# Kernel tuning notes

Measured on AMD Instinct MI355X. Metric: run time of the kernel, lower is better.

## Reference

```python
import jax, jax.numpy as jnp
import numpy as np

B, N, D, H, E = 4, 2048, 512, 8, 64  # batch, seq, model dim, heads, head dim
EPS = 1e-6
PAD = -2.0
NEG_INF = -1000000000.0
ROPE_MAX = 2048
ROPE_BASE = 10000.0


def compute_rope_rotations(dim, max_seq_len, base):
    inv_freq = 1.0 / base ** (jnp.arange(0, dim, 2, dtype=jnp.float32) / dim)
    pos = jnp.arange(max_seq_len, dtype=jnp.float32)
    freqs = pos[:, None] * inv_freq[None, :]          # (L, dim/2)
    freqs = jnp.repeat(freqs, 2, axis=-1)             # (L, dim)
    return jnp.cos(freqs), jnp.sin(freqs)


def apply_rope(x, cos, sin):
    # Faithful to the source: positions are indexed along AXIS 1 of x.
    # Since q/k have layout (b, h, n, e), axis 1 is the HEAD axis (source quirk).
    seq = x.shape[1]
    c = cos[:seq][None, :, None, :]
    s = sin[:seq][None, :, None, :]
    x1, x2 = x[..., 0::2], x[..., 1::2]
    ch, sh = c[..., 0::2], s[..., 0::2]
    r1 = x1 * ch - x2 * sh
    r2 = x1 * sh + x2 * ch
    return jnp.stack([r1, r2], axis=-1).reshape(x.shape)


def layer_norm(x, gamma, beta):
    mean = jnp.mean(x, axis=-1, keepdims=True)
    var = jnp.mean(jnp.square(x - mean), axis=-1, keepdims=True)
    return gamma * ((x - mean) / jnp.sqrt(var + EPS)) + beta


def setup_inputs() -> dict:
    key = jax.random.key(0)
    ks = jax.random.split(key, 10)
    x = jax.random.normal(ks[0], (B, N, D), dtype=jnp.float32)
    mask = jnp.where(jax.random.uniform(ks[1], (B, N)) < 0.1, PAD, 1.0).astype(jnp.float32)
    glorot_qkv = float(np.sqrt(6.0 / (D + E)))
    q_proj = jax.random.uniform(ks[2], (H, D, E), minval=-glorot_qkv, maxval=glorot_qkv, dtype=jnp.float32)
    k_proj = jax.random.uniform(ks[3], (H, D, E), minval=-glorot_qkv, maxval=glorot_qkv, dtype=jnp.float32)
    v_proj = jax.random.uniform(ks[4], (H, D, E), minval=-glorot_qkv, maxval=glorot_qkv, dtype=jnp.float32)
    g = jax.random.uniform(ks[5], (H, D, E), minval=-0.05, maxval=0.05, dtype=jnp.float32)
    glorot_out = float(np.sqrt(6.0 / (H * E + D)))
    out_w = jax.random.uniform(ks[6], (H * E, D), minval=-glorot_out, maxval=glorot_out, dtype=jnp.float32)
    out_b = jnp.zeros((D,), dtype=jnp.float32)
    gamma_in = jnp.ones((D,), dtype=jnp.float32)
    beta_in = jnp.zeros((D,), dtype=jnp.float32)
    gamma_out = jnp.ones((D,), dtype=jnp.float32)
    beta_out = jnp.zeros((D,), dtype=jnp.float32)
    rope_cos, rope_sin = compute_rope_rotations(E, ROPE_MAX, ROPE_BASE)
    return dict(x=x, mask=mask, q_proj=q_proj, k_proj=k_proj, v_proj=v_proj, g=g,
                gamma_in=gamma_in, beta_in=beta_in, gamma_out=gamma_out, beta_out=beta_out,
                out_w=out_w, out_b=out_b, rope_cos=rope_cos, rope_sin=rope_sin)


def reference(x, mask, q_proj, k_proj, v_proj, g, gamma_in, beta_in,
              gamma_out, beta_out, out_w, out_b, rope_cos, rope_sin):
    scale = 1.0 / jnp.sqrt(jnp.asarray(E, dtype=x.dtype))
    q_input = layer_norm(x, gamma_in, beta_in)          # self-attention: shared LN input
    mask_bin = jnp.where(mask == PAD, 0.0, 1.0).astype(x.dtype)  # (B, N)
    q = jnp.einsum('bnd,hde->bhne', q_input, q_proj)
    k = jnp.einsum('bmd,hde->bhme', q_input, k_proj)
    v = jnp.einsum('bmd,hde->bhme', q_input, v_proj)
    q = apply_rope(q, rope_cos, rope_sin)
    k = apply_rope(k, rope_cos, rope_sin)
    att = jnp.einsum('bhne,bhme->bhnm', q, k) * scale   # (B, H, N, N)
    amask = mask_bin[:, None, :, None] * mask_bin[:, None, None, :]  # (B,1,N,N)
    att = att + (1.0 - amask) * NEG_INF
    att = jax.nn.softmax(att, axis=-1) * amask
    out = jnp.einsum('bhnm,bhme->bhne', att, v)
    gate = jax.nn.sigmoid(jnp.einsum('bnd,hde->bhne', q_input, g))
    out = out * gate
    out = out.transpose(0, 2, 1, 3).reshape(x.shape[0], x.shape[1], H * E)
    out = out @ out_w + out_b
    out = out + x  # residual
    return layer_norm(out, gamma_out, beta_out)


if __name__ == '__main__':
    inp = setup_inputs()
    y = reference(**inp)
    print(y.shape, y.dtype)
```

## Files before the change

### kernel.cpp

```cpp
#include <hip/hip_runtime.h>
#include <math.h>

#define B_ 4
#define N_ 2048
#define D_ 512
#define H_ 8
#define E_ 64

constexpr float EPS = 1e-6f;
constexpr float PADV = -2.0f;
constexpr float SCL = 0.18033688011112043f;

typedef __attribute__((ext_vector_type(8))) __bf16 bf16x8;
typedef __attribute__((ext_vector_type(4))) float f32x4;

__device__ inline unsigned short f2bf(float f) {
  unsigned u = __builtin_bit_cast(unsigned, f);
  u += 0x7fffu + ((u >> 16) & 1u);
  return (unsigned short)(u >> 16);
}
__device__ inline float bf2f(unsigned short v) {
  unsigned u = ((unsigned)v) << 16;
  return __builtin_bit_cast(float, u);
}

__global__ __launch_bounds__(256) void prep_kernel(
    const float* __restrict__ qp, const float* __restrict__ kp,
    const float* __restrict__ vp, const float* __restrict__ gp,
    const float* __restrict__ ow, ushort* __restrict__ wT,
    ushort* __restrict__ owT) {
  __shared__ float Ls[64][65];
  int t = threadIdx.x;
  const float* src;
  ushort* dst;
  int src_ld, r0, c0;
  if (blockIdx.x < 256) {
    int set = blockIdx.x >> 6, tile = blockIdx.x & 63;
    int h = tile >> 3, dt = tile & 7;
    const float* w = set == 0 ? qp : set == 1 ? kp : set == 2 ? vp : gp;
    src = w + (size_t)h * 512 * 64;
    src_ld = 64;
    r0 = dt * 64;
    c0 = 0;
    dst = wT + ((size_t)set * 512 + h * 64) * 512;
  } else {
    int idx = blockIdx.x - 256;
    src = ow;
    src_ld = 512;
    r0 = (idx >> 3) * 64;
    c0 = (idx & 7) * 64;
    dst = owT;
  }
#pragma unroll
  for (int i = 0; i < 4; i++) {
    int id = t + i * 256;
    int r = id >> 4, c4 = (id & 15) * 4;
    float4 v = *(const float4*)(src + (size_t)(r0 + r) * src_ld + c0 + c4);
    Ls[r][c4] = v.x;
    Ls[r][c4 + 1] = v.y;
    Ls[r][c4 + 2] = v.z;
    Ls[r][c4 + 3] = v.w;
  }
  __syncthreads();
#pragma unroll
  for (int i = 0; i < 4; i++) {
    int id = t + i * 256;
    int c = id >> 4, r4 = (id & 15) * 4;
    ushort4 o;
    o.x = f2bf(Ls[r4][c]);
    o.y = f2bf(Ls[r4 + 1][c]);
    o.z = f2bf(Ls[r4 + 2][c]);
    o.w = f2bf(Ls[r4 + 3][c]);
    *(ushort4*)(dst + (size_t)(c0 + c) * 512 + r0 + r4) = o;
  }
}

__global__ __launch_bounds__(256) void ln_bf16_kernel(
    const float* __restrict__ x, const float* __restrict__ gamma,
    const float* __restrict__ beta, ushort* __restrict__ out) {
  int row = blockIdx.x;
  const float* xr = x + (size_t)row * D_;
  int c0 = threadIdx.x, c1 = threadIdx.x + 256;
  float v0 = xr[c0], v1 = xr[c1];
  __shared__ float red[8];
  int lane = threadIdx.x & 63, wid = threadIdx.x >> 6;
  float s = v0 + v1;
  for (int o = 32; o > 0; o >>= 1) s += __shfl_down(s, o, 64);
  if (lane == 0) red[wid] = s;
  __syncthreads();
  float mean = (red[0] + red[1] + red[2] + red[3]) * (1.0f / D_);
  float d0 = v0 - mean, d1 = v1 - mean;
  float sq = d0 * d0 + d1 * d1;
  for (int o = 32; o > 0; o >>= 1) sq += __shfl_down(sq, o, 64);
  if (lane == 0) red[4 + wid] = sq;
  __syncthreads();
  float var = (red[4] + red[5] + red[6] + red[7]) * (1.0f / D_);
  float rstd = rsqrtf(var + EPS);
  ushort* orow = out + (size_t)row * D_;
  orow[c0] = f2bf(gamma[c0] * (d0 * rstd) + beta[c0]);
  orow[c1] = f2bf(gamma[c1] * (d1 * rstd) + beta[c1]);
}

__global__ __launch_bounds__(256) void ln_kernel(
    const float* __restrict__ x, const float* __restrict__ gamma,
    const float* __restrict__ beta, float* __restrict__ out) {
  int row = blockIdx.x;
  const float* xr = x + (size_t)row * D_;
  int c0 = threadIdx.x, c1 = threadIdx.x + 256;
  float v0 = xr[c0], v1 = xr[c1];
  __shared__ float red[8];
  int lane = threadIdx.x & 63, wid = threadIdx.x >> 6;
  float s = v0 + v1;
  for (int o = 32; o > 0; o >>= 1) s += __shfl_down(s, o, 64);
  if (lane == 0) red[wid] = s;
  __syncthreads();
  float mean = (red[0] + red[1] + red[2] + red[3]) * (1.0f / D_);
  float d0 = v0 - mean, d1 = v1 - mean;
  float sq = d0 * d0 + d1 * d1;
  for (int o = 32; o > 0; o >>= 1) sq += __shfl_down(sq, o, 64);
  if (lane == 0) red[4 + wid] = sq;
  __syncthreads();
  float var = (red[4] + red[5] + red[6] + red[7]) * (1.0f / D_);
  float rstd = rsqrtf(var + EPS);
  float* orow = out + (size_t)row * D_;
  orow[c0] = gamma[c0] * (d0 * rstd) + beta[c0];
  orow[c1] = gamma[c1] * (d1 * rstd) + beta[c1];
}

__global__ __launch_bounds__(256) void proj_kernel(
    const ushort* __restrict__ xbf, const ushort* __restrict__ wT,
    const float* __restrict__ rope_cos, const float* __restrict__ rope_sin,
    ushort* __restrict__ qo, ushort* __restrict__ ko,
    ushort* __restrict__ vTo, ushort* __restrict__ go) {
  int tileM = blockIdx.x;
  int h = blockIdx.y & 7;
  int set = blockIdx.y >> 3;

  __shared__ ushort As[128 * 64];
  __shared__ ushort Bs[64 * 64];

  const int t = threadIdx.x;
  const int w = t >> 6;
  const int lane = t & 63;
  const int quad = lane >> 4;
  const int n15 = lane & 15;

  const ushort* wbase = wT + ((size_t)set * 512 + h * 64) * 512;
  const int bn0 = tileM * 128;

  f32x4 acc[2][4];
#pragma unroll
  for (int mb = 0; mb < 2; mb++)
#pragma unroll
    for (int tt = 0; tt < 4; tt++) acc[mb][tt] = (f32x4){0.f, 0.f, 0.f, 0.f};

  for (int k0 = 0; k0 < 512; k0 += 64) {
    __syncthreads();
#pragma unroll
    for (int i = 0; i < 4; i++) {
      int c = t + i * 256;
      int row = c >> 3, c8 = c & 7;
      *(uint4*)&As[(row << 6) + ((c8 ^ (row & 7)) << 3)] =
          *(const uint4*)(xbf + (size_t)(bn0 + row) * 512 + k0 + (c8 << 3));
    }
#pragma unroll
    for (int i = 0; i < 2; i++) {
      int c = t + i * 256;
      int row = c >> 3, c8 = c & 7;
      *(uint4*)&Bs[(row << 6) + ((c8 ^ (row & 7)) << 3)] =
          *(const uint4*)(wbase + (size_t)row * 512 + k0 + (c8 << 3));
    }
    __syncthreads();
#pragma unroll
    for (int kk = 0; kk < 2; kk++) {
      bf16x8 af[2], bfr[4];
#pragma unroll
      for (int mb = 0; mb < 2; mb++) {
        int m = 32 * w + 16 * mb + n15;
        af[mb] = __builtin_bit_cast(
            bf16x8,
            *(const uint4*)&As[(m << 6) + ((((kk << 2) + quad) ^ (m & 7)) << 3)]);
      }
#pragma unroll
      for (int tt = 0; tt < 4; tt++) {
        int n = 16 * tt + n15;
        bfr[tt] = __builtin_bit_cast(
            bf16x8,
            *(const uint4*)&Bs[(n << 6) + ((((kk << 2) + quad) ^ (n & 7)) << 3)]);
      }
#pragma unroll
      for (int mb = 0; mb < 2; mb++)
#pragma unroll
        for (int tt = 0; tt < 4; tt++)
          acc[mb][tt] = __builtin_amdgcn_mfma_f32_16x16x32_bf16(
              af[mb], bfr[tt], acc[mb][tt], 0, 0, 0);
    }
  }

  const int b = bn0 >> 11;
  const int n_base = bn0 & 2047;
  const int bh = b * H_ + h;
  const size_t bhN = (size_t)bh * N_;

  if (set <= 1) {
    ushort* dst = (set == 0) ? qo : ko;
    const float oscale = (set == 0) ? SCL : 1.0f;
    const float sgn = (n15 & 1) ? 1.f : -1.f;
#pragma unroll
    for (int tt = 0; tt < 4; tt++) {
      int e = 16 * tt + n15;
      float cv = rope_cos[(h << 6) + e];
      float sv = rope_sin[(h << 6) + e];
#pragma unroll
      for (int mb = 0; mb < 2; mb++) {
#pragma unroll
        for (int r = 0; r < 4; r++) {
          float xv = acc[mb][tt][r];
          float pv = __shfl_xor(xv, 1, 64);
          float ov = (xv * cv + sgn * pv * sv) * oscale;
          int n = n_base + 32 * w + 16 * mb + 4 * quad + r;
          dst[((bhN + n) << 6) + e] = f2bf(ov);
        }
      }
    }
  } else if (set == 2) {
#pragma unroll
    for (int tt = 0; tt < 4; tt++) {
      int e = 16 * tt + n15;
#pragma unroll
      for (int mb = 0; mb < 2; mb++) {
        int n0 = n_base + 32 * w + 16 * mb + 4 * quad;
        ushort4 pk;
        pk.x = f2bf(acc[mb][tt][0]);
        pk.y = f2bf(acc[mb][tt][1]);
        pk.z = f2bf(acc[mb][tt][2]);
        pk.w = f2bf(acc[mb][tt][3]);
        *(ushort4*)(vTo + ((size_t)(bh * 64 + e)) * N_ + n0) = pk;
      }
    }
  } else {
#pragma unroll
    for (int tt = 0; tt < 4; tt++) {
      int e = 16 * tt + n15;
#pragma unroll
      for (int mb = 0; mb < 2; mb++) {
#pragma unroll
        for (int r = 0; r < 4; r++) {
          int n = n_base + 32 * w + 16 * mb + 4 * quad + r;
          float sv = 1.0f / (1.0f + __expf(-acc[mb][tt][r]));
          go[((bhN + n) << 6) + e] = f2bf(sv);
        }
      }
    }
  }
}

__global__ __launch_bounds__(512, 4) void attn_kernel(
    const ushort* __restrict__ qb, const ushort* __restrict__ kb,
    const ushort* __restrict__ vT, const ushort* __restrict__ gb,
    const float* __restrict__ mask, ushort* __restrict__ out) {
  int qt = blockIdx.x;
  int bh = blockIdx.y;
  int b = bh >> 3, h = bh & 7;

  __shared__ uint Ksu[64 * 32];
  __shared__ uint Vtsu[66 * 32];
  __shared__ uint Pw[8 * 16 * 36];
  __shared__ __align__(16) float kmb[64];

  const int t = threadIdx.x;
  const int w = t >> 6;
  const int lane = t & 63;
  const int quad = lane >> 4;
  const int n15 = lane & 15;
  const int sw = n15 & 7;

  const size_t bhN = (size_t)bh * N_;
  const size_t bN = (size_t)b * N_;
  const int q0 = qt * 128 + 16 * w;

  bf16x8 qf[2];
  {
    const ushort* qrow = qb + ((bhN + q0 + n15) << 6);
#pragma unroll
    for (int hf = 0; hf < 2; hf++)
      qf[hf] =
          __builtin_bit_cast(bf16x8, *(const uint4*)(qrow + 32 * hf + (quad << 3)));
  }

  if (t < 32) Vtsu[64 * 32 + t] = 0x3f803f80u;

  f32x4 O[4], O5;
  O5 = (f32x4){0.f, 0.f, 0.f, 0.f};
#pragma unroll
  for (int tt = 0; tt < 4; tt++) O[tt] = (f32x4){0.f, 0.f, 0.f, 0.f};

  uint* Pq = &Pw[w * 576];

  for (int m0 = 0; m0 < N_; m0 += 64) {
    __syncthreads();
    {
      int row = t >> 3, c8 = t & 7;
      int dst = row * 32 + ((c8 ^ (row & 7)) << 2);
      *(uint4*)&Ksu[dst] =
          *(const uint4*)(kb + ((bhN + m0 + row) << 6) + (c8 << 3));
      *(uint4*)&Vtsu[dst] =
          *(const uint4*)(vT + (size_t)(bh * 64 + row) * N_ + m0 + (c8 << 3));
    }
    if (t < 16) {
      f32x4 mv = *(const f32x4*)(mask + bN + m0 + 4 * t);
      f32x4 bias;
#pragma unroll
      for (int j = 0; j < 4; j++) bias[j] = (mv[j] == PADV) ? -1e9f : 0.f;
      *(f32x4*)&kmb[4 * t] = bias;
    }
    __syncthreads();

    f32x4 st[4];
#pragma unroll
    for (int tt = 0; tt < 4; tt++)
      st[tt] = *(const f32x4*)&kmb[16 * tt + 4 * quad];
#pragma unroll
    for (int hf = 0; hf < 2; hf++) {
#pragma unroll
      for (int tt = 0; tt < 4; tt++) {
        bf16x8 kf = __builtin_bit_cast(
            bf16x8, *(const uint4*)&Ksu[(16 * tt + n15) * 32 +
                                        (((quad + 4 * hf) ^ sw) << 2)]);
        st[tt] =
            __builtin_amdgcn_mfma_f32_16x16x32_bf16(kf, qf[hf], st[tt], 0, 0, 0);
      }
    }

    int rowb = n15 * 36;
#pragma unroll
    for (int tt = 0; tt < 4; tt++) {
      uint u0 = __builtin_bit_cast(
                    uint, __builtin_exp2f(fminf(st[tt][0], 60.f))) + 0x8000u;
      uint u1 = __builtin_bit_cast(
                    uint, __builtin_exp2f(fminf(st[tt][1], 60.f))) + 0x8000u;
      uint u2 = __builtin_bit_cast(
                    uint, __builtin_exp2f(fminf(st[tt][2], 60.f))) + 0x8000u;
      uint u3 = __builtin_bit_cast(
                    uint, __builtin_exp2f(fminf(st[tt][3], 60.f))) + 0x8000u;
      int a = rowb + ((2 * tt + (quad >> 1)) << 2) + ((quad & 1) << 1);
      Pq[a] = __builtin_amdgcn_perm(u1, u0, 0x07060302u);
      Pq[a + 1] = __builtin_amdgcn_perm(u3, u2, 0x07060302u);
    }
    __asm__ volatile("" ::: "memory");

#pragma unroll
    for (int hf = 0; hf < 2; hf++) {
      bf16x8 pf = __builtin_bit_cast(
          bf16x8, *(const uint4*)&Pq[n15 * 36 + ((quad + 4 * hf) << 2)]);
      bf16x8 lf = __builtin_bit_cast(
          bf16x8, *(const uint4*)&Vtsu[64 * 32 + ((quad + 4 * hf) << 2)]);
      O5 = __builtin_amdgcn_mfma_f32_16x16x32_bf16(pf, lf, O5, 0, 0, 0);
#pragma unroll
      for (int tt = 0; tt < 4; tt++) {
        bf16x8 vf = __builtin_bit_cast(
            bf16x8, *(const uint4*)&Vtsu[(16 * tt + n15) * 32 +
                                         (((quad + 4 * hf) ^ sw) << 2)]);
        O[tt] =
            __builtin_amdgcn_mfma_f32_16x16x32_bf16(pf, vf, O[tt], 0, 0, 0);
      }
    }
  }

#pragma unroll
  for (int r = 0; r < 4; r++) {
    int n = q0 + 4 * quad + r;
    float qm = (mask[bN + n] == PADV) ? 0.f : 1.f;
    float inv = qm / fmaxf(O5[r], 1e-30f);
    const ushort* grow = gb + ((bhN + n) << 6);
    ushort* orow = out + ((bN + n) << 9) + (h << 6);
#pragma unroll
    for (int tt = 0; tt < 4; tt++) {
      int e = 16 * tt + n15;
      orow[e] = f2bf(O[tt][r] * inv * bf2f(grow[e]));
    }
  }
}

__global__ __launch_bounds__(256) void outproj_kernel(
    const ushort* __restrict__ ain, const ushort* __restrict__ owT,
    const float* __restrict__ bias, const float* __restrict__ xres,
    float* __restrict__ out) {
  int tileM = blockIdx.x;
  int cc0 = blockIdx.y * 64;

  __shared__ ushort As[128 * 64];
  __shared__ ushort Bs[64 * 64];

  const int t = threadIdx.x;
  const int w = t >> 6;
  const int lane = t & 63;
  const int quad = lane >> 4;
  const int n15 = lane & 15;

  const ushort* wbase = owT + (size_t)cc0 * 512;
  const int bn0 = tileM * 128;

  f32x4 acc[2][4];
#pragma unroll
  for (int mb = 0; mb < 2; mb++)
#pragma unroll
    for (int tt = 0; tt < 4; tt++) acc[mb][tt] = (f32x4){0.f, 0.f, 0.f, 0.f};

  for (int k0 = 0; k0 < 512; k0 += 64) {
    __syncthreads();
#pragma unroll
    for (int i = 0; i < 4; i++) {
      int c = t + i * 256;
      int row = c >> 3, c8 = c & 7;
      *(uint4*)&As[(row << 6) + ((c8 ^ (row & 7)) << 3)] =
          *(const uint4*)(ain + (size_t)(bn0 + row) * 512 + k0 + (c8 << 3));
    }
#pragma unroll
    for (int i = 0; i < 2; i++) {
      int c = t + i * 256;
      int row = c >> 3, c8 = c & 7;
      *(uint4*)&Bs[(row << 6) + ((c8 ^ (row & 7)) << 3)] =
          *(const uint4*)(wbase + (size_t)row * 512 + k0 + (c8 << 3));
    }
    __syncthreads();
#pragma unroll
    for (int kk = 0; kk < 2; kk++) {
      bf16x8 af[2], bfr[4];
#pragma unroll
      for (int mb = 0; mb < 2; mb++) {
        int m = 32 * w + 16 * mb + n15;
        af[mb] = __builtin_bit_cast(
            bf16x8,
            *(const uint4*)&As[(m << 6) + ((((kk << 2) + quad) ^ (m & 7)) << 3)]);
      }
#pragma unroll
      for (int tt = 0; tt < 4; tt++) {
        int n = 16 * tt + n15;
        bfr[tt] = __builtin_bit_cast(
            bf16x8,
            *(const uint4*)&Bs[(n << 6) + ((((kk << 2) + quad) ^ (n & 7)) << 3)]);
      }
#pragma unroll
      for (int mb = 0; mb < 2; mb++)
#pragma unroll
        for (int tt = 0; tt < 4; tt++)
          acc[mb][tt] = __builtin_amdgcn_mfma_f32_16x16x32_bf16(
              af[mb], bfr[tt], acc[mb][tt], 0, 0, 0);
    }
  }

#pragma unroll
  for (int tt = 0; tt < 4; tt++) {
    int c = cc0 + 16 * tt + n15;
    float bv = bias[c];
#pragma unroll
    for (int mb = 0; mb < 2; mb++) {
#pragma unroll
      for (int r = 0; r < 4; r++) {
        size_t row = bn0 + 32 * w + 16 * mb + 4 * quad + r;
        out[row * 512 + c] = acc[mb][tt][r] + bv + xres[row * 512 + c];
      }
    }
  }
}

extern "C" void kernel_launch(void* const* d_in, const int* in_sizes, int n_in,
                              void* d_out, int out_size, void* d_ws,
                              size_t ws_size, hipStream_t stream) {
  (void)in_sizes; (void)n_in; (void)out_size; (void)ws_size;
  const float* x = (const float*)d_in[0];
  const float* mask = (const float*)d_in[1];
  const float* q_proj = (const float*)d_in[2];
  const float* k_proj = (const float*)d_in[3];
  const float* v_proj = (const float*)d_in[4];
  const float* g = (const float*)d_in[5];
  const float* gamma_in = (const float*)d_in[6];
  const float* beta_in = (const float*)d_in[7];
  const float* gamma_out = (const float*)d_in[8];
  const float* beta_out = (const float*)d_in[9];
  const float* out_w = (const float*)d_in[10];
  const float* out_b = (const float*)d_in[11];
  const float* rope_cos = (const float*)d_in[12];
  const float* rope_sin = (const float*)d_in[13];

  char* p = (char*)d_ws;
  ushort* xbf   = (ushort*)p; p += (size_t)8 << 20;
  ushort* wT    = (ushort*)p; p += (size_t)2 << 20;
  ushort* owT   = (ushort*)p; p += (size_t)1 << 20;
  ushort* qb16  = (ushort*)p; p += (size_t)8 << 20;
  ushort* kb16  = (ushort*)p; p += (size_t)8 << 20;
  ushort* vT16  = (ushort*)p; p += (size_t)8 << 20;
  ushort* gate  = (ushort*)p; p += (size_t)8 << 20;
  ushort* attnb = (ushort*)p; p += (size_t)8 << 20;
  float* ypre   = (float*)p;  p += (size_t)16 << 20;

  prep_kernel<<<320, 256, 0, stream>>>(q_proj, k_proj, v_proj, g, out_w, wT,
                                       owT);

  ln_bf16_kernel<<<B_ * N_, 256, 0, stream>>>(x, gamma_in, beta_in, xbf);

  dim3 gp(64, 32);
  proj_kernel<<<gp, 256, 0, stream>>>(xbf, wT, rope_cos, rope_sin, qb16, kb16,
                                      vT16, gate);

  dim3 ga(16, 32);
  attn_kernel<<<ga, 512, 0, stream>>>(qb16, kb16, vT16, gate, mask, attnb);

  dim3 go(64, 8);
  outproj_kernel<<<go, 256, 0, stream>>>(attnb, owT, out_b, x, ypre);

  ln_kernel<<<B_ * N_, 256, 0, stream>>>(ypre, gamma_out, beta_out,
                                         (float*)d_out);
}
```

Baseline: 216.1 us.

## Split attention KV range across two warp groups with 32-row query tiles per warp

Each warp now handles two 16-row query blocks (32 rows), so every K/V fragment read from shared memory feeds two MFMAs instead of one. The 8 warps form two groups that each process half of the key sequence with their own K/V tiles, and the partial outputs and row sums are combined through shared memory at the end. The ones vector for the row-sum MFMA moves into registers instead of a shared-memory row. This halves shared-memory fragment traffic per MFMA and the loop count per block, at the cost of more accumulator registers, an extra reduction step, and an epilogue where half the warps sit idle.

```diff
diff --git a/kernel.cpp b/kernel.cpp
--- a/kernel.cpp
+++ b/kernel.cpp
@@ -13,6 +13,7 @@
 
 typedef __attribute__((ext_vector_type(8))) __bf16 bf16x8;
 typedef __attribute__((ext_vector_type(4))) float f32x4;
+typedef __attribute__((ext_vector_type(8))) unsigned short u16x8;
 
 __device__ inline unsigned short f2bf(float f) {
   unsigned u = __builtin_bit_cast(unsigned, f);
@@ -263,121 +264,184 @@
   int bh = blockIdx.y;
   int b = bh >> 3, h = bh & 7;
 
-  __shared__ uint Ksu[64 * 32];
-  __shared__ uint Vtsu[66 * 32];
-  __shared__ uint Pw[8 * 16 * 36];
-  __shared__ __align__(16) float kmb[64];
+  __shared__ __align__(16) uint arena[12928];
 
   const int t = threadIdx.x;
   const int w = t >> 6;
+  const int grp = w >> 2;
+  const int gw = w & 3;
   const int lane = t & 63;
   const int quad = lane >> 4;
   const int n15 = lane & 15;
   const int sw = n15 & 7;
+  const int tg = t & 255;
+
+  uint* Ks = &arena[grp * 4096];
+  uint* Vts = &arena[grp * 4096 + 2048];
+  uint* Pq = &arena[8192 + w * 576];
+  float* kmbf = (float*)&arena[12800];
 
   const size_t bhN = (size_t)bh * N_;
   const size_t bN = (size_t)b * N_;
-  const int q0 = qt * 128 + 16 * w;
-
-  bf16x8 qf[2];
+  const int q0 = qt * 128 + 32 * gw;
+  const int koff = grp << 10;
+
+  bf16x8 qf[2][2];
+#pragma unroll
+  for (int mb = 0; mb < 2; mb++) {
+    const ushort* qrow = qb + ((bhN + q0 + 16 * mb + n15) << 6);
+#pragma unroll
+    for (int hf = 0; hf < 2; hf++)
+      qf[mb][hf] = __builtin_bit_cast(
+          bf16x8, *(const uint4*)(qrow + 32 * hf + (quad << 3)));
+  }
+
+  bf16x8 ones;
   {
-    const ushort* qrow = qb + ((bhN + q0 + n15) << 6);
-#pragma unroll
-    for (int hf = 0; hf < 2; hf++)
-      qf[hf] =
-          __builtin_bit_cast(bf16x8, *(const uint4*)(qrow + 32 * hf + (quad << 3)));
-  }
-
-  if (t < 32) Vtsu[64 * 32 + t] = 0x3f803f80u;
-
-  f32x4 O[4], O5;
-  O5 = (f32x4){0.f, 0.f, 0.f, 0.f};
-#pragma unroll
-  for (int tt = 0; tt < 4; tt++) O[tt] = (f32x4){0.f, 0.f, 0.f, 0.f};
-
-  uint* Pq = &Pw[w * 576];
-
-  for (int m0 = 0; m0 < N_; m0 += 64) {
+    u16x8 ou;
+#pragma unroll
+    for (int j = 0; j < 8; j++) ou[j] = 0x3F80;
+    ones = __builtin_bit_cast(bf16x8, ou);
+  }
+
+  f32x4 O[2][4], O5[2];
+#pragma unroll
+  for (int mb = 0; mb < 2; mb++) {
+    O5[mb] = (f32x4){0.f, 0.f, 0.f, 0.f};
+#pragma unroll
+    for (int tt = 0; tt < 4; tt++) O[mb][tt] = (f32x4){0.f, 0.f, 0.f, 0.f};
+  }
+
+  for (int it = 0; it < 16; it++) {
+    int m0 = koff + (it << 6);
     __syncthreads();
-    {
-      int row = t >> 3, c8 = t & 7;
+#pragma unroll
+    for (int i = 0; i < 2; i++) {
+      int idx = tg + (i << 8);
+      int row = idx >> 3, c8 = idx & 7;
       int dst = row * 32 + ((c8 ^ (row & 7)) << 2);
-      *(uint4*)&Ksu[dst] =
+      *(uint4*)&Ks[dst] =
           *(const uint4*)(kb + ((bhN + m0 + row) << 6) + (c8 << 3));
-      *(uint4*)&Vtsu[dst] =
+      *(uint4*)&Vts[dst] =
           *(const uint4*)(vT + (size_t)(bh * 64 + row) * N_ + m0 + (c8 << 3));
     }
-    if (t < 16) {
-      f32x4 mv = *(const f32x4*)(mask + bN + m0 + 4 * t);
+    if (tg < 16) {
+      f32x4 mv = *(const f32x4*)(mask + bN + m0 + 4 * tg);
       f32x4 bias;
 #pragma unroll
       for (int j = 0; j < 4; j++) bias[j] = (mv[j] == PADV) ? -1e9f : 0.f;
-      *(f32x4*)&kmb[4 * t] = bias;
+      *(f32x4*)&kmbf[(grp << 6) + 4 * tg] = bias;
     }
     __syncthreads();
 
-    f32x4 st[4];
+    f32x4 bias[4];
 #pragma unroll
     for (int tt = 0; tt < 4; tt++)
-      st[tt] = *(const f32x4*)&kmb[16 * tt + 4 * quad];
+      bias[tt] = *(const f32x4*)&kmbf[(grp << 6) + 16 * tt + 4 * quad];
+
+    f32x4 st[2][4];
+#pragma unroll
+    for (int mb = 0; mb < 2; mb++)
+#pragma unroll
+      for (int tt = 0; tt < 4; tt++) st[mb][tt] = bias[tt];
 #pragma unroll
     for (int hf = 0; hf < 2; hf++) {
 #pragma unroll
       for (int tt = 0; tt < 4; tt++) {
         bf16x8 kf = __builtin_bit_cast(
-            bf16x8, *(const uint4*)&Ksu[(16 * tt + n15) * 32 +
-                                        (((quad + 4 * hf) ^ sw) << 2)]);
-        st[tt] =
-            __builtin_amdgcn_mfma_f32_16x16x32_bf16(kf, qf[hf], st[tt], 0, 0, 0);
-      }
-    }
-
-    int rowb = n15 * 36;
-#pragma unroll
-    for (int tt = 0; tt < 4; tt++) {
-      uint u0 = __builtin_bit_cast(
-                    uint, __builtin_exp2f(fminf(st[tt][0], 60.f))) + 0x8000u;
-      uint u1 = __builtin_bit_cast(
-                    uint, __builtin_exp2f(fminf(st[tt][1], 60.f))) + 0x8000u;
-      uint u2 = __builtin_bit_cast(
-                    uint, __builtin_exp2f(fminf(st[tt][2], 60.f))) + 0x8000u;
-      uint u3 = __builtin_bit_cast(
-                    uint, __builtin_exp2f(fminf(st[tt][3], 60.f))) + 0x8000u;
-      int a = rowb + ((2 * tt + (quad >> 1)) << 2) + ((quad & 1) << 1);
-      Pq[a] = __builtin_amdgcn_perm(u1, u0, 0x07060302u);
-      Pq[a + 1] = __builtin_amdgcn_perm(u3, u2, 0x07060302u);
-    }
-    __asm__ volatile("" ::: "memory");
+            bf16x8, *(const uint4*)&Ks[(16 * tt + n15) * 32 +
+                                       (((quad + 4 * hf) ^ sw) << 2)]);
+        st[0][tt] = __builtin_amdgcn_mfma_f32_16x16x32_bf16(kf, qf[0][hf],
+                                                            st[0][tt], 0, 0, 0);
+        st[1][tt] = __builtin_amdgcn_mfma_f32_16x16x32_bf16(kf, qf[1][hf],
+                                                            st[1][tt], 0, 0, 0);
+      }
+    }
+
+    bf16x8 pf[2][2];
+#pragma unroll
+    for (int mb = 0; mb < 2; mb++) {
+      int rowb = n15 * 36;
+#pragma unroll
+      for (int tt = 0; tt < 4; tt++) {
+        uint u0 = __builtin_bit_cast(
+                      uint, __builtin_exp2f(fminf(st[mb][tt][0], 60.f))) +
+                  0x8000u;
+        uint u1 = __builtin_bit_cast(
+                      uint, __builtin_exp2f(fminf(st[mb][tt][1], 60.f))) +
+                  0x8000u;
+        uint u2 = __builtin_bit_cast(
+                      uint, __builtin_exp2f(fminf(st[mb][tt][2], 60.f))) +
+                  0x8000u;
+        uint u3 = __builtin_bit_cast(
+                      uint, __builtin_exp2f(fminf(st[mb][tt][3], 60.f))) +
+                  0x8000u;
+        int a = rowb + ((2 * tt + (quad >> 1)) << 2) + ((quad & 1) << 1);
+        Pq[a] = __builtin_amdgcn_perm(u1, u0, 0x07060302u);
+        Pq[a + 1] = __builtin_amdgcn_perm(u3, u2, 0x07060302u);
+      }
+      __asm__ volatile("" ::: "memory");
+#pragma unroll
+      for (int hf = 0; hf < 2; hf++)
+        pf[mb][hf] = __builtin_bit_cast(
+            bf16x8, *(const uint4*)&Pq[n15 * 36 + ((quad + 4 * hf) << 2)]);
+      __asm__ volatile("" ::: "memory");
+    }
 
 #pragma unroll
     for (int hf = 0; hf < 2; hf++) {
-      bf16x8 pf = __builtin_bit_cast(
-          bf16x8, *(const uint4*)&Pq[n15 * 36 + ((quad + 4 * hf) << 2)]);
-      bf16x8 lf = __builtin_bit_cast(
-          bf16x8, *(const uint4*)&Vtsu[64 * 32 + ((quad + 4 * hf) << 2)]);
-      O5 = __builtin_amdgcn_mfma_f32_16x16x32_bf16(pf, lf, O5, 0, 0, 0);
+      O5[0] = __builtin_amdgcn_mfma_f32_16x16x32_bf16(pf[0][hf], ones, O5[0],
+                                                      0, 0, 0);
+      O5[1] = __builtin_amdgcn_mfma_f32_16x16x32_bf16(pf[1][hf], ones, O5[1],
+                                                      0, 0, 0);
 #pragma unroll
       for (int tt = 0; tt < 4; tt++) {
         bf16x8 vf = __builtin_bit_cast(
-            bf16x8, *(const uint4*)&Vtsu[(16 * tt + n15) * 32 +
-                                         (((quad + 4 * hf) ^ sw) << 2)]);
-        O[tt] =
-            __builtin_amdgcn_mfma_f32_16x16x32_bf16(pf, vf, O[tt], 0, 0, 0);
-      }
-    }
-  }
-
-#pragma unroll
-  for (int r = 0; r < 4; r++) {
-    int n = q0 + 4 * quad + r;
-    float qm = (mask[bN + n] == PADV) ? 0.f : 1.f;
-    float inv = qm / fmaxf(O5[r], 1e-30f);
-    const ushort* grow = gb + ((bhN + n) << 6);
-    ushort* orow = out + ((bN + n) << 9) + (h << 6);
-#pragma unroll
-    for (int tt = 0; tt < 4; tt++) {
-      int e = 16 * tt + n15;
-      orow[e] = f2bf(O[tt][r] * inv * bf2f(grow[e]));
+            bf16x8, *(const uint4*)&Vts[(16 * tt + n15) * 32 +
+                                        (((quad + 4 * hf) ^ sw) << 2)]);
+        O[0][tt] = __builtin_amdgcn_mfma_f32_16x16x32_bf16(pf[0][hf], vf,
+                                                           O[0][tt], 0, 0, 0);
+        O[1][tt] = __builtin_amdgcn_mfma_f32_16x16x32_bf16(pf[1][hf], vf,
+                                                           O[1][tt], 0, 0, 0);
+      }
+    }
+  }
+
+  __syncthreads();
+  f32x4* cbuf = (f32x4*)arena;
+  int ci = (gw * 64 + lane) * 10;
+  if (grp == 1) {
+#pragma unroll
+    for (int mb = 0; mb < 2; mb++)
+#pragma unroll
+      for (int tt = 0; tt < 4; tt++) cbuf[ci + mb * 4 + tt] = O[mb][tt];
+    cbuf[ci + 8] = O5[0];
+    cbuf[ci + 9] = O5[1];
+  }
+  __syncthreads();
+  if (grp == 0) {
+#pragma unroll
+    for (int mb = 0; mb < 2; mb++)
+#pragma unroll
+      for (int tt = 0; tt < 4; tt++) O[mb][tt] += cbuf[ci + mb * 4 + tt];
+    O5[0] += cbuf[ci + 8];
+    O5[1] += cbuf[ci + 9];
+
+#pragma unroll
+    for (int mb = 0; mb < 2; mb++) {
+#pragma unroll
+      for (int r = 0; r < 4; r++) {
+        int n = q0 + 16 * mb + 4 * quad + r;
+        float qm = (mask[bN + n] == PADV) ? 0.f : 1.f;
+        float inv = qm / fmaxf(O5[mb][r], 1e-30f);
+        const ushort* grow = gb + ((bhN + n) << 6);
+        ushort* orow = out + ((bN + n) << 9) + (h << 6);
+#pragma unroll
+        for (int tt = 0; tt < 4; tt++) {
+          int e = 16 * tt + n15;
+          orow[e] = f2bf(O[mb][tt][r] * inv * bf2f(grow[e]));
+        }
+      }
     }
   }
 }
```

Measured after the change: 223.8 us. 3.6% more time.
